# Kernel optimization log

Measured on AMD Instinct MI355X. Metric: run time of the kernel, lower is better.

The kernel has to match this reference:

```python
import jax, jax.numpy as jnp
import numpy as np

B, IN, H, HEADS, W, P = 512, 512, 1024, 16, 32, 64
EPS = 1e-5

def _pe(w, p, dtype=jnp.float32):
    # sinusoidal positional encoding over the attention window, [w, p]
    pos = jnp.arange(w, dtype=dtype)[:, None]
    div = jnp.exp(-jnp.arange(0, p, 2, dtype=dtype) * (np.log(10000.0) / p))
    ang = pos * div[None, :]
    pe = jnp.zeros((w, p), dtype)
    pe = pe.at[:, 0::2].set(jnp.sin(ang))
    pe = pe.at[:, 1::2].set(jnp.cos(ang))
    return pe

def _bn(x, g, b, m, v):
    # BatchNorm1d in eval mode (running stats)
    return (x - m) * (g / jnp.sqrt(v + EPS)) + b

def setup_inputs():
    key = jax.random.key(0)
    ks = iter(jax.random.split(key, 40))
    s = 1.0 / np.sqrt(H)  # init_parameters('pytorch_default'): U(-1/sqrt(H), 1/sqrt(H))
    u = lambda shape: jax.random.uniform(next(ks), shape, jnp.float32, -s, s)
    rn = lambda shape: jax.random.normal(next(ks), shape, jnp.float32)
    return {
        "x": rn((B, IN)),
        "prev_hidden": rn((B, H)),
        "prev_cell": rn((B, H)),
        "past_cells": rn((W, B, H)),
        "W_ih": u((4 * H, IN)), "b_ih": u((4 * H,)),
        "W_hh": u((4 * H, H)),
        "W_q": u((H, IN + H)), "b_q": u((H,)),
        "W_ac": u((4 * H, H)), "b_ac": u((4 * H,)),
        "Wq_a": u((H, H)), "bq_a": u((H,)),
        "Wk_a": u((H, H + P)), "bk_a": u((H,)),
        "Wv_a": u((H, H + P)), "bv_a": u((H,)),
        "Wo_a": u((H, H)), "bo_a": u((H,)),
        "bn_attn_gamma": u((H,)), "bn_attn_beta": u((H,)),
        "bn_attn_mean": jnp.zeros((H,)), "bn_attn_var": jnp.ones((H,)),
        "bn_post_gamma": u((H,)), "bn_post_beta": u((H,)),
        "bn_post_mean": jnp.zeros((H,)), "bn_post_var": jnp.ones((H,)),
    }

def reference(x, prev_hidden, prev_cell, past_cells, W_ih, b_ih, W_hh, W_q, b_q, W_ac, b_ac, Wq_a, bq_a, Wk_a, bk_a, Wv_a, bv_a, Wo_a, bo_a, bn_attn_gamma, bn_attn_beta, bn_attn_mean, bn_attn_var, bn_post_gamma, bn_post_beta, bn_post_mean, bn_post_var):
    dk = H // HEADS
    # Q = elu(Wq * concat(x, h) + b)
    q = jax.nn.elu(jnp.concatenate([x, prev_hidden], -1) @ W_q.T + b_q)      # [B,H]
    # K = V = window of past cell states (+ positional encoding on features)
    vals = jnp.transpose(past_cells, (1, 0, 2))                              # [B,W,H]
    pe = jnp.broadcast_to(_pe(W, P)[None], (vals.shape[0], W, P))
    kv = jnp.concatenate([vals, pe], -1)                                     # [B,W,H+P]
    Q = (q @ Wq_a.T + bq_a).reshape(-1, HEADS, dk)                           # [B,h,dk]
    K = jax.nn.elu(kv @ Wk_a.T + bk_a).reshape(-1, W, HEADS, dk)             # activation_on_keys_and_values
    V = jax.nn.elu(kv @ Wv_a.T + bv_a).reshape(-1, W, HEADS, dk)
    scores = jnp.einsum('bhd,bwhd->bhw', Q, K) / np.sqrt(dk)
    ctx = jnp.einsum('bhw,bwhd->bhd', jax.nn.softmax(scores, -1), V).reshape(-1, H)
    attn = jax.nn.elu(ctx @ Wo_a.T + bo_a)                                   # [B,H]
    attn = _bn(attn, bn_attn_gamma, bn_attn_beta, bn_attn_mean, bn_attn_var)
    # 'residual' mode: Wx*x + Wh*h + Wa*a + b  (note: original returns pre-BN value)
    pre = x @ W_ih.T + b_ih + prev_hidden @ W_hh.T + attn @ W_ac.T + b_ac    # [B,4H]
    iv = jnp.tanh(pre[:, :H])
    gates = jax.nn.sigmoid(pre[:, H:])
    f, i, o = gates[:, :H], gates[:, H:2 * H], gates[:, 2 * H:]
    cell = iv * i + prev_cell * f
    hidden = _bn(o * jax.nn.elu(cell), bn_post_gamma, bn_post_beta, bn_post_mean, bn_post_var)
    return hidden
```

## Files before the change

kernel.cpp:

```cpp
#include <hip/hip_runtime.h>
#include <hip/hip_bf16.h>

typedef __attribute__((ext_vector_type(8))) short s16x8;
typedef __attribute__((ext_vector_type(8))) unsigned short u16x8;
typedef __attribute__((ext_vector_type(4))) float f32x4;

__device__ __forceinline__ float bf2f(unsigned short u) {
  union { unsigned int i; float f; } v; v.i = ((unsigned int)u) << 16; return v.f;
}
__device__ __forceinline__ unsigned short f2bf(float f) {
  union { float f; unsigned int i; } v; v.f = f;
  unsigned int u = v.i;
  unsigned int r = (u + 0x7fffu + ((u >> 16) & 1u)) >> 16;
  return (unsigned short)r;
}
__device__ __forceinline__ float eluf(float x) { return x > 0.f ? x : __expf(x) - 1.f; }
__device__ __forceinline__ float sigf(float x) { return 1.f / (1.f + __expf(-x)); }
__device__ __forceinline__ float tanhfast(float x) {
  float ax = fminf(fabsf(x), 15.f);
  float e2 = __expf(2.f * ax);
  float t = (e2 - 1.f) / (e2 + 1.f);
  return x < 0.f ? -t : t;
}

__device__ __forceinline__ void gl_lds16(const unsigned short* g, unsigned short* l) {
  __builtin_amdgcn_global_load_lds(
      (const __attribute__((address_space(1))) void*)g,
      (__attribute__((address_space(3))) void*)l, 16, 0, 0);
}

struct CP {
  const float *pcs, *W_ih, *W_hh, *W_ac, *W_q, *Wq_a, *Wo_a, *Wk_a, *Wv_a, *x, *ph;
  const float *b_ih, *b_ac, *bk, *bv;
  const float *g1, *be1, *m1, *v1, *g2, *be2, *m2, *v2;
  unsigned short *A_pc, *W6, *Wq, *Wqa, *Woa, *Wkv, *A6;
  float *peb, *bias6, *s1, *t1, *s2, *t2;
};

__global__ __launch_bounds__(256)
void cast_all(CP p) {
  int c = blockIdx.x * 256 + threadIdx.x;
  const float* src; unsigned short* dst; int row, col, ldd;
  if (c < 2097152) {
    row = c >> 7; col = (c & 127) << 3;
    src = p.pcs + (size_t)row * 1024 + col; dst = p.A_pc; ldd = 1024;
  } else if (c < 3407872) {
    int i = c - 2097152; row = i / 320; col = (i - row * 320) << 3;
    dst = p.W6; ldd = 2560;
    src = (col < 512)  ? p.W_ih + (size_t)row * 512 + col
        : (col < 1536) ? p.W_hh + (size_t)row * 1024 + (col - 512)
                       : p.W_ac + (size_t)row * 1024 + (col - 1536);
  } else if (c < 3604480) {
    int i = c - 3407872; row = i / 192; col = (i - row * 192) << 3;
    src = p.W_q + (size_t)row * 1536 + col; dst = p.Wq; ldd = 1536;
  } else if (c < 3735552) {
    int i = c - 3604480; row = i >> 7; col = (i & 127) << 3;
    src = p.Wq_a + (size_t)row * 1024 + col; dst = p.Wqa; ldd = 1024;
  } else if (c < 3866624) {
    int i = c - 3735552; row = i >> 7; col = (i & 127) << 3;
    src = p.Wo_a + (size_t)row * 1024 + col; dst = p.Woa; ldd = 1024;
  } else if (c < 4128768) {
    int i = c - 3866624; row = i >> 7; col = (i & 127) << 3;
    src = (row < 1024) ? p.Wk_a + (size_t)row * 1088 + col
                       : p.Wv_a + (size_t)(row - 1024) * 1088 + col;
    dst = p.Wkv; ldd = 1024;
  } else if (c < 4227072) {
    int i = c - 4128768; row = i / 192; col = (i - row * 192) << 3;
    src = (col < 512) ? p.x + (size_t)row * 512 + col
                      : p.ph + (size_t)row * 1024 + (col - 512);
    dst = p.A6; ldd = 2560;
  } else if (c < 4292608) {
    int idx = c - 4227072;
    int w = idx >> 11, n = idx & 2047;
    const float* Wrow =
        ((n < 1024) ? (p.Wk_a + (size_t)n * 1088)
                    : (p.Wv_a + (size_t)(n - 1024) * 1088)) + 1024;
    float accv = (n < 1024) ? p.bk[n] : p.bv[n - 1024];
    const float c0 = 0.14391157f;
#pragma unroll
    for (int j = 0; j < 32; ++j) {
      float ang = (float)w * __expf(-(2.f * j) * c0);
      accv += __sinf(ang) * Wrow[2 * j] + __cosf(ang) * Wrow[2 * j + 1];
    }
    p.peb[idx] = accv;
    return;
  } else {
    int i = c - 4292608;
    if (i < 4096) p.bias6[i] = p.b_ih[i] + p.b_ac[i];
    if (i < 1024) {
      float sa = p.g1[i] * rsqrtf(p.v1[i] + 1e-5f);
      p.s1[i] = sa; p.t1[i] = p.be1[i] - p.m1[i] * sa;
      float sp = p.g2[i] * rsqrtf(p.v2[i] + 1e-5f);
      p.s2[i] = sp; p.t2[i] = p.be2[i] - p.m2[i] * sp;
    }
    return;
  }
  f32x4 v0 = *(const f32x4*)src;
  f32x4 v1 = *(const f32x4*)(src + 4);
  u16x8 r;
  r[0] = f2bf(v0.x); r[1] = f2bf(v0.y); r[2] = f2bf(v0.z); r[3] = f2bf(v0.w);
  r[4] = f2bf(v1.x); r[5] = f2bf(v1.y); r[6] = f2bf(v1.z); r[7] = f2bf(v1.w);
  int sc = col ^ ((row & 7) << 3);
  *(u16x8*)(dst + (size_t)row * ldd + sc) = r;
}

struct GP2 {
  const unsigned short* A; long lda;
  const unsigned short* B; long ldb;
  const float* bias;
  const float* bnS; const float* bnT;
  float* of; unsigned short* ob;
  int N, K;
};

template<int BM, int BN, int EPI, int ACT>
__global__ __launch_bounds__(256)
void gemm2(GP2 p) {
  __shared__ unsigned short sA[BM * 64];
  __shared__ unsigned short sB[BN * 64];
  const int tid = threadIdx.x, lane = tid & 63, wid = tid >> 6;
  const int col0 = blockIdx.x * BN, row0 = blockIdx.y * BM;
  constexpr int WRS = BM / 2, WCS = BN / 2;
  constexpr int MI = WRS / 16, NI = WCS / 16;
  const int wr = (wid >> 1) * WRS, wc = (wid & 1) * WCS;
  const int g = lane >> 4, lr = lane & 15;
  f32x4 acc[MI][NI] = {};

  for (int kb = 0; kb < p.K; kb += 64) {
    __syncthreads();
#pragma unroll
    for (int ps = 0; ps < (BM * 8) / 256; ++ps) {
      int chunk = ps * 256 + tid;
      int r = chunk >> 3, c8 = chunk & 7;
      gl_lds16(p.A + (size_t)(row0 + r) * p.lda + kb + c8 * 8, &sA[chunk * 8]);
    }
#pragma unroll
    for (int ps = 0; ps < (BN * 8) / 256; ++ps) {
      int chunk = ps * 256 + tid;
      int r = chunk >> 3, c8 = chunk & 7;
      gl_lds16(p.B + (size_t)(col0 + r) * p.ldb + kb + c8 * 8, &sB[chunk * 8]);
    }
    __syncthreads();
#pragma unroll
    for (int kk = 0; kk < 64; kk += 32) {
      s16x8 af[MI], bf_[NI];
#pragma unroll
      for (int i = 0; i < MI; ++i) {
        int ar = wr + i * 16 + lr;
        int sl = ((kk >> 3) + g) ^ (ar & 7);
        af[i] = *(const s16x8*)(&sA[(ar * 8 + sl) * 8]);
      }
#pragma unroll
      for (int i = 0; i < NI; ++i) {
        int br = wc + i * 16 + lr;
        int sl = ((kk >> 3) + g) ^ (br & 7);
        bf_[i] = *(const s16x8*)(&sB[(br * 8 + sl) * 8]);
      }
#pragma unroll
      for (int mi = 0; mi < MI; ++mi)
#pragma unroll
        for (int ni = 0; ni < NI; ++ni)
          acc[mi][ni] = __builtin_amdgcn_mfma_f32_16x16x32_bf16(
              af[mi], bf_[ni], acc[mi][ni], 0, 0, 0);
    }
  }

#pragma unroll
  for (int mi = 0; mi < MI; ++mi) {
#pragma unroll
    for (int ni = 0; ni < NI; ++ni) {
#pragma unroll
      for (int rg = 0; rg < 4; ++rg) {
        int rr = row0 + wr + mi * 16 + g * 4 + rg;
        int cc = col0 + wc + ni * 16 + lr;
        float v = acc[mi][ni][rg] + p.bias[cc];
        if constexpr (ACT) v = eluf(v);
        if constexpr (EPI == 0) {
          p.of[(size_t)rr * p.N + cc] = v;
        } else if constexpr (EPI == 1) {
          p.ob[(size_t)rr * p.N + (cc ^ ((rr & 7) << 3))] = f2bf(v);
        } else {
          v = v * p.bnS[cc] + p.bnT[cc];
          p.ob[(size_t)rr * 2560 + ((1536 + cc) ^ ((rr & 7) << 3))] = f2bf(v);
        }
      }
    }
  }
}

__global__ __launch_bounds__(256)
void gkv_attn(const unsigned short* __restrict__ A_pc,
              const unsigned short* __restrict__ Wkv,
              const float* __restrict__ peb,
              const float* __restrict__ Qf,
              unsigned short* __restrict__ ctx) {
  __shared__ unsigned short smem[2 * 128 * 64];
  __shared__ float prs[4][32];
  __shared__ float qs[4][64];
  unsigned short* sA = smem;
  unsigned short* sB = smem + 128 * 64;

  int id = blockIdx.x;
  int nid = (id & 7) * 256 + (id >> 3);
  const int h = nid & 15, bg = nid >> 4;
  const int b0 = bg * 4;

  const int tid = threadIdx.x, lane = tid & 63, wid = tid >> 6;
  const int wr = (wid >> 1) * 64, wc = (wid & 1) * 64;
  const int g = lane >> 4, lr = lane & 15;
  f32x4 acc[4][4] = {};

  for (int kb = 0; kb < 1024; kb += 64) {
    __syncthreads();
#pragma unroll
    for (int ps = 0; ps < 4; ++ps) {
      int chunk = ps * 256 + tid;
      int r = chunk >> 3, c8 = chunk & 7;
      int w = r >> 2;
      int srow = w * 512 + b0 + (r & 3);
      int xf = (r & 7) ^ (srow & 7);
      gl_lds16(A_pc + (size_t)srow * 1024 + kb + ((c8 ^ xf) << 3), &sA[chunk * 8]);
    }
#pragma unroll
    for (int ps = 0; ps < 4; ++ps) {
      int chunk = ps * 256 + tid;
      int r = chunk >> 3, c8 = chunk & 7;
      int n = h * 64 + r + (r >= 64 ? 960 : 0);
      gl_lds16(Wkv + (size_t)n * 1024 + kb + (c8 << 3), &sB[chunk * 8]);
    }
    __syncthreads();
#pragma unroll
    for (int kk = 0; kk < 64; kk += 32) {
      s16x8 af[4], bf_[4];
#pragma unroll
      for (int i = 0; i < 4; ++i) {
        int ar = wr + i * 16 + lr;
        int sl = ((kk >> 3) + g) ^ (ar & 7);
        af[i] = *(const s16x8*)(&sA[(ar * 8 + sl) * 8]);
        int br = wc + i * 16 + lr;
        int sl2 = ((kk >> 3) + g) ^ (br & 7);
        bf_[i] = *(const s16x8*)(&sB[(br * 8 + sl2) * 8]);
      }
#pragma unroll
      for (int mi = 0; mi < 4; ++mi)
#pragma unroll
        for (int ni = 0; ni < 4; ++ni)
          acc[mi][ni] = __builtin_amdgcn_mfma_f32_16x16x32_bf16(
              af[mi], bf_[ni], acc[mi][ni], 0, 0, 0);
    }
  }
  __syncthreads();

  unsigned short (*kv)[128] = (unsigned short(*)[128])smem;
#pragma unroll
  for (int mi = 0; mi < 4; ++mi) {
#pragma unroll
    for (int ni = 0; ni < 4; ++ni) {
#pragma unroll
      for (int rg = 0; rg < 4; ++rg) {
        int rr = wr + mi * 16 + g * 4 + rg;
        int cc = wc + ni * 16 + lr;
        int w = rr >> 2;
        int gcol = h * 64 + cc + (cc >= 64 ? 960 : 0);
        float v = acc[mi][ni][rg] + peb[w * 2048 + gcol];
        v = v > 0.f ? v : __expf(v) - 1.f;
        kv[rr][cc ^ ((rr & 7) << 3)] = f2bf(v);
      }
    }
  }
  qs[wid][lane] = Qf[(size_t)(b0 + wid) * 1024 + h * 64 + lane];
  __syncthreads();

  const int wv = wid;
  const int w = lane & 31, half = lane >> 5;
  float s = 0.f;
  {
    int r = w * 4 + wv;
    int swz = r & 7;
#pragma unroll
    for (int jj = 0; jj < 4; ++jj) {
      u16x8 kx = *(const u16x8*)(&kv[r][((half * 4 + jj) ^ swz) << 3]);
#pragma unroll
      for (int e = 0; e < 8; ++e)
        s += qs[wv][half * 32 + jj * 8 + e] * bf2f(kx[e]);
    }
  }
  s += __shfl_xor(s, 32);
  s *= 0.125f;
  float mx = s;
#pragma unroll
  for (int off = 16; off; off >>= 1) mx = fmaxf(mx, __shfl_xor(mx, off));
  float e = __expf(s - mx);
  float sum = e;
#pragma unroll
  for (int off = 16; off; off >>= 1) sum += __shfl_xor(sum, off);
  if (lane < 32) prs[wv][lane] = e / sum;

  float c = 0.f;
  const int d = lane;
#pragma unroll 8
  for (int w2 = 0; w2 < 32; ++w2) {
    int r = w2 * 4 + wv;
    c += prs[wv][w2] * bf2f(kv[r][(64 + d) ^ ((r & 7) << 3)]);
  }
  int b = b0 + wv;
  ctx[(size_t)b * 1024 + ((h * 64 + d) ^ ((b & 7) << 3))] = f2bf(c);
}

__global__ __launch_bounds__(256)
void final_k(const float* __restrict__ pre, const float* __restrict__ pcell,
             const float* __restrict__ s2, const float* __restrict__ t2,
             float* __restrict__ out) {
  int i = blockIdx.x * 256 + threadIdx.x;
  int j = i & 1023;
  const float* pm = pre + (size_t)(i >> 10) * 4096;
  float iv = tanhfast(pm[j]);
  float f  = sigf(pm[1024 + j]);
  float ii = sigf(pm[2048 + j]);
  float o  = sigf(pm[3072 + j]);
  float cell = iv * ii + pcell[i] * f;
  float ec = cell > 0.f ? cell : __expf(cell) - 1.f;
  out[i] = (o * ec) * s2[j] + t2[j];
}

extern "C" void kernel_launch(void* const* d_in, const int* in_sizes, int n_in,
                              void* d_out, int out_size, void* d_ws, size_t ws_size,
                              hipStream_t stream) {
  (void)in_sizes; (void)n_in; (void)out_size; (void)ws_size;
  const float* x     = (const float*)d_in[0];
  const float* ph    = (const float*)d_in[1];
  const float* pcell = (const float*)d_in[2];
  const float* pcs   = (const float*)d_in[3];
  const float* W_ih  = (const float*)d_in[4];
  const float* b_ih  = (const float*)d_in[5];
  const float* W_hh  = (const float*)d_in[6];
  const float* W_q   = (const float*)d_in[7];
  const float* b_q   = (const float*)d_in[8];
  const float* W_ac  = (const float*)d_in[9];
  const float* b_ac  = (const float*)d_in[10];
  const float* Wq_a  = (const float*)d_in[11];
  const float* bq_a  = (const float*)d_in[12];
  const float* Wk_a  = (const float*)d_in[13];
  const float* bk_a  = (const float*)d_in[14];
  const float* Wv_a  = (const float*)d_in[15];
  const float* bv_a  = (const float*)d_in[16];
  const float* Wo_a  = (const float*)d_in[17];
  const float* bo_a  = (const float*)d_in[18];

  char* wp = (char*)d_ws;
  auto alloc = [&](size_t bytes) {
    char* r = wp; wp += (bytes + 255) & ~(size_t)255; return r;
  };
  unsigned short* A_pc  = (unsigned short*)alloc((size_t)16384 * 1024 * 2);
  unsigned short* W6    = (unsigned short*)alloc((size_t)4096 * 2560 * 2);
  unsigned short* Wq    = (unsigned short*)alloc((size_t)1024 * 1536 * 2);
  unsigned short* Wqa   = (unsigned short*)alloc((size_t)1024 * 1024 * 2);
  unsigned short* Woa   = (unsigned short*)alloc((size_t)1024 * 1024 * 2);
  unsigned short* Wkv   = (unsigned short*)alloc((size_t)2048 * 1024 * 2);
  unsigned short* A6    = (unsigned short*)alloc((size_t)512 * 2560 * 2);
  unsigned short* q_bf  = (unsigned short*)alloc((size_t)512 * 1024 * 2);
  float*          Qf    = (float*)alloc((size_t)512 * 1024 * 4);
  unsigned short* ctxbf = (unsigned short*)alloc((size_t)512 * 1024 * 2);
  float*          pre   = (float*)alloc((size_t)512 * 4096 * 4);
  float*          peb   = (float*)alloc((size_t)32 * 2048 * 4);
  float*          bias6 = (float*)alloc((size_t)4096 * 4);
  float*          s1    = (float*)alloc((size_t)1024 * 4);
  float*          t1    = (float*)alloc((size_t)1024 * 4);
  float*          s2    = (float*)alloc((size_t)1024 * 4);
  float*          t2    = (float*)alloc((size_t)1024 * 4);

  {
    CP cp = {};
    cp.pcs = pcs; cp.W_ih = W_ih; cp.W_hh = W_hh; cp.W_ac = W_ac; cp.W_q = W_q;
    cp.Wq_a = Wq_a; cp.Wo_a = Wo_a; cp.Wk_a = Wk_a; cp.Wv_a = Wv_a;
    cp.x = x; cp.ph = ph;
    cp.b_ih = b_ih; cp.b_ac = b_ac; cp.bk = bk_a; cp.bv = bv_a;
    cp.g1 = (const float*)d_in[19]; cp.be1 = (const float*)d_in[20];
    cp.m1 = (const float*)d_in[21]; cp.v1 = (const float*)d_in[22];
    cp.g2 = (const float*)d_in[23]; cp.be2 = (const float*)d_in[24];
    cp.m2 = (const float*)d_in[25]; cp.v2 = (const float*)d_in[26];
    cp.A_pc = A_pc; cp.W6 = W6; cp.Wq = Wq; cp.Wqa = Wqa; cp.Woa = Woa;
    cp.Wkv = Wkv; cp.A6 = A6;
    cp.peb = peb; cp.bias6 = bias6; cp.s1 = s1; cp.t1 = t1; cp.s2 = s2; cp.t2 = t2;
    cast_all<<<16784, 256, 0, stream>>>(cp);
  }

  {
    GP2 p = {};
    p.A = A6; p.lda = 2560; p.B = Wq; p.ldb = 1536;
    p.bias = b_q; p.ob = q_bf; p.N = 1024; p.K = 1536;
    gemm2<64, 64, 1, 1><<<dim3(16, 8), 256, 0, stream>>>(p);
  }
  {
    GP2 p = {};
    p.A = q_bf; p.lda = 1024; p.B = Wqa; p.ldb = 1024;
    p.bias = bq_a; p.of = Qf; p.N = 1024; p.K = 1024;
    gemm2<64, 64, 0, 0><<<dim3(16, 8), 256, 0, stream>>>(p);
  }
  gkv_attn<<<2048, 256, 0, stream>>>(A_pc, Wkv, peb, Qf, ctxbf);
  {
    GP2 p = {};
    p.A = ctxbf; p.lda = 1024; p.B = Woa; p.ldb = 1024;
    p.bias = bo_a; p.bnS = s1; p.bnT = t1; p.ob = A6; p.N = 1024; p.K = 1024;
    gemm2<64, 64, 3, 1><<<dim3(16, 8), 256, 0, stream>>>(p);
  }
  {
    GP2 p = {};
    p.A = A6; p.lda = 2560; p.B = W6; p.ldb = 2560;
    p.bias = bias6; p.of = pre; p.N = 4096; p.K = 2560;
    gemm2<64, 128, 0, 0><<<dim3(32, 8), 256, 0, stream>>>(p);
  }
  final_k<<<2048, 256, 0, stream>>>(pre, pcell, s2, t2, (float*)d_out);
}
```

Measured before the change: 381.1 us.

## Triple-buffer GEMM loads, fuse LSTM gate epilogue, interleave gate rows

The GEMM is rewritten as a triple-buffered pipeline: loads for tile t+2 are issued asynchronously, explicit vmcnt waits and barriers are placed around them, and the old single-stage load-sync loop goes away. The W6 weight rows and bias6 are permuted so that each group of four adjacent output columns holds the i/f/g/o gates of one hidden unit. This lets the final GEMM compute the LSTM cell and BN directly in its epilogue using lane shuffles, and the pre buffer and the final_k kernel are removed. The smaller GEMMs switch to 32x64 tiles to launch more blocks, and the big GEMM moves to 64x64 tiles. The added cost is triple-buffered LDS occupancy and an epilogue in which only one lane in four does the gate arithmetic.

```diff
diff --git a/kernel.cpp b/kernel.cpp
--- a/kernel.cpp
+++ b/kernel.cpp
@@ -27,6 +27,19 @@
   __builtin_amdgcn_global_load_lds(
       (const __attribute__((address_space(1))) void*)g,
       (__attribute__((address_space(3))) void*)l, 16, 0, 0);
+}
+
+template<int N> __device__ __forceinline__ void waitv() {
+  if constexpr (N == 0) asm volatile("s_waitcnt vmcnt(0)" ::: "memory");
+  else if constexpr (N == 3) asm volatile("s_waitcnt vmcnt(3)" ::: "memory");
+  else if constexpr (N == 4) asm volatile("s_waitcnt vmcnt(4)" ::: "memory");
+  else if constexpr (N == 6) asm volatile("s_waitcnt vmcnt(6)" ::: "memory");
+  else if constexpr (N == 8) asm volatile("s_waitcnt vmcnt(8)" ::: "memory");
+}
+__device__ __forceinline__ void sbar() {
+  __builtin_amdgcn_sched_barrier(0);
+  __builtin_amdgcn_s_barrier();
+  __builtin_amdgcn_sched_barrier(0);
 }
 
 struct CP {
@@ -45,11 +58,12 @@
     row = c >> 7; col = (c & 127) << 3;
     src = p.pcs + (size_t)row * 1024 + col; dst = p.A_pc; ldd = 1024;
   } else if (c < 3407872) {
-    int i = c - 2097152; row = i / 320; col = (i - row * 320) << 3;
+    int i = c - 2097152; int orow = i / 320; col = (i - orow * 320) << 3;
     dst = p.W6; ldd = 2560;
-    src = (col < 512)  ? p.W_ih + (size_t)row * 512 + col
-        : (col < 1536) ? p.W_hh + (size_t)row * 1024 + (col - 512)
-                       : p.W_ac + (size_t)row * 1024 + (col - 1536);
+    src = (col < 512)  ? p.W_ih + (size_t)orow * 512 + col
+        : (col < 1536) ? p.W_hh + (size_t)orow * 1024 + (col - 512)
+                       : p.W_ac + (size_t)orow * 1024 + (col - 1536);
+    row = (orow & 1023) * 4 + (orow >> 10);
   } else if (c < 3604480) {
     int i = c - 3407872; row = i / 192; col = (i - row * 192) << 3;
     src = p.W_q + (size_t)row * 1536 + col; dst = p.Wq; ldd = 1536;
@@ -86,7 +100,7 @@
     return;
   } else {
     int i = c - 4292608;
-    if (i < 4096) p.bias6[i] = p.b_ih[i] + p.b_ac[i];
+    if (i < 4096) p.bias6[(i & 1023) * 4 + (i >> 10)] = p.b_ih[i] + p.b_ac[i];
     if (i < 1024) {
       float sa = p.g1[i] * rsqrtf(p.v1[i] + 1e-5f);
       p.s1[i] = sa; p.t1[i] = p.be1[i] - p.m1[i] * sa;
@@ -109,15 +123,17 @@
   const unsigned short* B; long ldb;
   const float* bias;
   const float* bnS; const float* bnT;
+  const float* pcell;
   float* of; unsigned short* ob;
   int N, K;
 };
 
 template<int BM, int BN, int EPI, int ACT>
 __global__ __launch_bounds__(256)
-void gemm2(GP2 p) {
-  __shared__ unsigned short sA[BM * 64];
-  __shared__ unsigned short sB[BN * 64];
+void sgemm(GP2 p) {
+  constexpr int LA = (BM * 8) / 256, LB = (BN * 8) / 256, L = LA + LB;
+  __shared__ unsigned short sA[3][BM * 64];
+  __shared__ unsigned short sB[3][BN * 64];
   const int tid = threadIdx.x, lane = tid & 63, wid = tid >> 6;
   const int col0 = blockIdx.x * BN, row0 = blockIdx.y * BM;
   constexpr int WRS = BM / 2, WCS = BN / 2;
@@ -126,21 +142,21 @@
   const int g = lane >> 4, lr = lane & 15;
   f32x4 acc[MI][NI] = {};
 
-  for (int kb = 0; kb < p.K; kb += 64) {
-    __syncthreads();
-#pragma unroll
-    for (int ps = 0; ps < (BM * 8) / 256; ++ps) {
-      int chunk = ps * 256 + tid;
+  auto stage = [&](int buf, int kb) {
+#pragma unroll
+    for (int i = 0; i < LA; ++i) {
+      int chunk = i * 256 + tid;
       int r = chunk >> 3, c8 = chunk & 7;
-      gl_lds16(p.A + (size_t)(row0 + r) * p.lda + kb + c8 * 8, &sA[chunk * 8]);
-    }
-#pragma unroll
-    for (int ps = 0; ps < (BN * 8) / 256; ++ps) {
-      int chunk = ps * 256 + tid;
+      gl_lds16(p.A + (size_t)(row0 + r) * p.lda + kb + c8 * 8, &sA[buf][chunk * 8]);
+    }
+#pragma unroll
+    for (int i = 0; i < LB; ++i) {
+      int chunk = i * 256 + tid;
       int r = chunk >> 3, c8 = chunk & 7;
-      gl_lds16(p.B + (size_t)(col0 + r) * p.ldb + kb + c8 * 8, &sB[chunk * 8]);
-    }
-    __syncthreads();
+      gl_lds16(p.B + (size_t)(col0 + r) * p.ldb + kb + c8 * 8, &sB[buf][chunk * 8]);
+    }
+  };
+  auto compute = [&](int buf) {
 #pragma unroll
     for (int kk = 0; kk < 64; kk += 32) {
       s16x8 af[MI], bf_[NI];
@@ -148,13 +164,13 @@
       for (int i = 0; i < MI; ++i) {
         int ar = wr + i * 16 + lr;
         int sl = ((kk >> 3) + g) ^ (ar & 7);
-        af[i] = *(const s16x8*)(&sA[(ar * 8 + sl) * 8]);
+        af[i] = *(const s16x8*)(&sA[buf][(ar * 8 + sl) * 8]);
       }
 #pragma unroll
       for (int i = 0; i < NI; ++i) {
         int br = wc + i * 16 + lr;
         int sl = ((kk >> 3) + g) ^ (br & 7);
-        bf_[i] = *(const s16x8*)(&sB[(br * 8 + sl) * 8]);
+        bf_[i] = *(const s16x8*)(&sB[buf][(br * 8 + sl) * 8]);
       }
 #pragma unroll
       for (int mi = 0; mi < MI; ++mi)
@@ -163,6 +179,25 @@
           acc[mi][ni] = __builtin_amdgcn_mfma_f32_16x16x32_bf16(
               af[mi], bf_[ni], acc[mi][ni], 0, 0, 0);
     }
+  };
+
+  const int nt = p.K >> 6;
+  stage(0, 0);
+  stage(1, 64);
+  int bufc = 0;
+  for (int t = 0; t < nt; ++t) {
+    if (t + 2 < nt) {
+      stage(bufc >= 1 ? bufc - 1 : bufc + 2, (t + 2) << 6);
+      waitv<2 * L>();
+    } else if (t + 1 < nt) {
+      waitv<L>();
+    } else {
+      waitv<0>();
+    }
+    sbar();
+    compute(bufc);
+    sbar();
+    bufc = bufc < 2 ? bufc + 1 : 0;
   }
 
 #pragma unroll
@@ -179,9 +214,25 @@
           p.of[(size_t)rr * p.N + cc] = v;
         } else if constexpr (EPI == 1) {
           p.ob[(size_t)rr * p.N + (cc ^ ((rr & 7) << 3))] = f2bf(v);
-        } else {
+        } else if constexpr (EPI == 3) {
           v = v * p.bnS[cc] + p.bnT[cc];
           p.ob[(size_t)rr * 2560 + ((1536 + cc) ^ ((rr & 7) << 3))] = f2bf(v);
+        } else {
+          int base = lane & ~3;
+          float g0 = __shfl(v, base);
+          float g1 = __shfl(v, base | 1);
+          float g2v = __shfl(v, base | 2);
+          float g3 = __shfl(v, base | 3);
+          if ((lane & 3) == 0) {
+            int j = cc >> 2;
+            float iv = tanhfast(g0);
+            float fg = sigf(g1);
+            float ig = sigf(g2v);
+            float og = sigf(g3);
+            float cell = iv * ig + p.pcell[(size_t)rr * 1024 + j] * fg;
+            float ec = cell > 0.f ? cell : __expf(cell) - 1.f;
+            p.of[(size_t)rr * 1024 + j] = (og * ec) * p.bnS[j] + p.bnT[j];
+          }
         }
       }
     }
@@ -305,22 +356,6 @@
   }
   int b = b0 + wv;
   ctx[(size_t)b * 1024 + ((h * 64 + d) ^ ((b & 7) << 3))] = f2bf(c);
-}
-
-__global__ __launch_bounds__(256)
-void final_k(const float* __restrict__ pre, const float* __restrict__ pcell,
-             const float* __restrict__ s2, const float* __restrict__ t2,
-             float* __restrict__ out) {
-  int i = blockIdx.x * 256 + threadIdx.x;
-  int j = i & 1023;
-  const float* pm = pre + (size_t)(i >> 10) * 4096;
-  float iv = tanhfast(pm[j]);
-  float f  = sigf(pm[1024 + j]);
-  float ii = sigf(pm[2048 + j]);
-  float o  = sigf(pm[3072 + j]);
-  float cell = iv * ii + pcell[i] * f;
-  float ec = cell > 0.f ? cell : __expf(cell) - 1.f;
-  out[i] = (o * ec) * s2[j] + t2[j];
 }
 
 extern "C" void kernel_launch(void* const* d_in, const int* in_sizes, int n_in,
@@ -361,7 +396,6 @@
   unsigned short* q_bf  = (unsigned short*)alloc((size_t)512 * 1024 * 2);
   float*          Qf    = (float*)alloc((size_t)512 * 1024 * 4);
   unsigned short* ctxbf = (unsigned short*)alloc((size_t)512 * 1024 * 2);
-  float*          pre   = (float*)alloc((size_t)512 * 4096 * 4);
   float*          peb   = (float*)alloc((size_t)32 * 2048 * 4);
   float*          bias6 = (float*)alloc((size_t)4096 * 4);
   float*          s1    = (float*)alloc((size_t)1024 * 4);
@@ -389,26 +423,26 @@
     GP2 p = {};
     p.A = A6; p.lda = 2560; p.B = Wq; p.ldb = 1536;
     p.bias = b_q; p.ob = q_bf; p.N = 1024; p.K = 1536;
-    gemm2<64, 64, 1, 1><<<dim3(16, 8), 256, 0, stream>>>(p);
+    sgemm<32, 64, 1, 1><<<dim3(16, 16), 256, 0, stream>>>(p);
   }
   {
     GP2 p = {};
     p.A = q_bf; p.lda = 1024; p.B = Wqa; p.ldb = 1024;
     p.bias = bq_a; p.of = Qf; p.N = 1024; p.K = 1024;
-    gemm2<64, 64, 0, 0><<<dim3(16, 8), 256, 0, stream>>>(p);
+    sgemm<32, 64, 0, 0><<<dim3(16, 16), 256, 0, stream>>>(p);
   }
   gkv_attn<<<2048, 256, 0, stream>>>(A_pc, Wkv, peb, Qf, ctxbf);
   {
     GP2 p = {};
     p.A = ctxbf; p.lda = 1024; p.B = Woa; p.ldb = 1024;
     p.bias = bo_a; p.bnS = s1; p.bnT = t1; p.ob = A6; p.N = 1024; p.K = 1024;
-    gemm2<64, 64, 3, 1><<<dim3(16, 8), 256, 0, stream>>>(p);
+    sgemm<32, 64, 3, 1><<<dim3(16, 16), 256, 0, stream>>>(p);
   }
   {
     GP2 p = {};
     p.A = A6; p.lda = 2560; p.B = W6; p.ldb = 2560;
-    p.bias = bias6; p.of = pre; p.N = 4096; p.K = 2560;
-    gemm2<64, 128, 0, 0><<<dim3(32, 8), 256, 0, stream>>>(p);
-  }
-  final_k<<<2048, 256, 0, stream>>>(pre, pcell, s2, t2, (float*)d_out);
-}
+    p.bias = bias6; p.bnS = s2; p.bnT = t2; p.pcell = pcell;
+    p.of = (float*)d_out; p.N = 4096; p.K = 2560;
+    sgemm<64, 64, 4, 0><<<dim3(64, 8), 256, 0, stream>>>(p);
+  }
+}
```

New measurement: 375.5 us. About the same (-1.5%).
